# Kernel optimization log

Hardware: AMD Instinct MI355X
Metric: run time of the kernel (lower is better)

The kernel has to match this reference:

```python
import jax, jax.numpy as jnp
import numpy as np

# The torch code implements pixel shifts via bmm with sparse permutation
# matrices: T[i,i+1]=1. bmm(x, T) moves column j-1 -> j (shift right, zero col 0);
# bmm(x, T^T) shifts left; bmm(T, x) moves row j+1 -> j (shift up, zero last row);
# bmm(T^T, x) shifts down. We implement these directly as pad+slice gathers.

def _shift_right(x):  # [B,H,W]
    return jnp.pad(x[:, :, :-1], ((0, 0), (0, 0), (1, 0)))

def _shift_left(x):
    return jnp.pad(x[:, :, 1:], ((0, 0), (0, 0), (0, 1)))

def _shift_up(x):
    return jnp.pad(x[:, 1:, :], ((0, 0), (0, 1), (0, 0)))

def _shift_down(x):
    return jnp.pad(x[:, :-1, :], ((0, 0), (1, 0), (0, 0)))

def _bce_sum(p, t):
    # torch.nn.BCELoss(reduction='sum') clamps log terms at -100
    logp = jnp.clip(jnp.log(p), -100.0, None)
    log1mp = jnp.clip(jnp.log1p(-p), -100.0, None)
    return -jnp.sum(t * logp + (1.0 - t) * log1mp)

def setup_inputs() -> dict:
    key = jax.random.key(0)
    k1, k2, k3 = jax.random.split(key, 3)
    B, C, H, W = 16, 8, 512, 512
    c_map = jax.random.normal(k1, (B, C, H, W), dtype=jnp.float32)
    target = jax.random.bernoulli(k2, 0.5, (B, 1, H, W)).astype(jnp.float32)
    con_target = jax.random.bernoulli(k3, 0.5, (B, C, H, W)).astype(jnp.float32)
    return {"c_map": c_map, "target": target, "con_target": con_target}

def reference(c_map, target, con_target):
    p = jax.nn.sigmoid(c_map)  # [B,8,H,W]

    sum_conn = jnp.sum(con_target, axis=1)  # [B,H,W]
    edge = ((sum_conn < 8.0) & (sum_conn > 0.0)).astype(p.dtype)

    c0, c1, c2, c3 = p[:, 0], p[:, 1], p[:, 2], p[:, 3]
    c4, c5, c6, c7 = p[:, 4], p[:, 5], p[:, 6], p[:, 7]

    right = _shift_right(c4)
    left = _shift_left(c3)
    left_bottom = _shift_left(_shift_down(c5))
    right_above = _shift_right(_shift_up(c2))
    left_above = _shift_left(_shift_up(c0))
    bottom = _shift_down(c6)
    up = _shift_up(c1)
    right_bottom = _shift_right(_shift_down(c7))

    a1 = c3 * right
    a2 = c4 * left
    a3 = c1 * bottom
    a4 = c6 * up
    a5 = c2 * left_bottom
    a6 = c5 * right_above
    a7 = c0 * right_bottom
    a8 = c7 * left_above

    vote_out = jnp.stack([a7, a3, a5, a1, a2, a6, a4, a8], axis=1)  # [B,8,H,W]

    glo_map = jnp.mean(vote_out, axis=1)       # [B,H,W]
    pred_mask_min = jnp.min(vote_out, axis=1)  # [B,H,W]
    decouple_map = glo_map * (1.0 - edge) + (1.0 - pred_mask_min) * edge

    de_loss = _bce_sum(decouple_map[:, None], target)
    conmap_l = _bce_sum(p, con_target)
    bimap_l = _bce_sum(vote_out, con_target)
    return 0.8 * conmap_l + de_loss + 0.2 * bimap_l
```

## Files before the change

### kernel.cpp

```cpp
#include <hip/hip_runtime.h>
#include <math.h>

#define NB 16
#define NC 8
#define HH 512
#define WW 512
#define HW (HH * WW)
#define CHW (NC * HW)

typedef const __attribute__((address_space(1))) void* gvp;
typedef __attribute__((address_space(3))) void*       lvp;

__device__ __forceinline__ float sigf(float x) {
    return __fdividef(1.0f, 1.0f + __expf(-x));
}

__device__ __forceinline__ float bce_term(float t, float p) {
    float q = (t > 0.5f) ? p : (1.0f - p);
    return -fmaxf(__logf(q), -100.0f);
}

__device__ __forceinline__ void ld4(const float* p, float* o) {
    float4 v = *(const float4*)p;
    o[0] = v.x; o[1] = v.y; o[2] = v.z; o[3] = v.w;
}

__global__ __launch_bounds__(256) void bicon_loss_kernel(
    const float* __restrict__ c_map,
    const float* __restrict__ target,
    const float* __restrict__ con_target,
    float* __restrict__ out)
{
    __shared__ float lds[22][WW];

    const int b    = blockIdx.x >> 8;
    const int h0   = (blockIdx.x & 255) << 1;
    const int tid  = threadIdx.x;
    const int wave = tid >> 6;
    const int lane = tid & 63;

    for (int s = wave; s < 44; s += 4) {
        const int plane = s >> 1, half = s & 1;
        int ch, rel;
        if      (plane < 3)  { ch = 5 + plane;  rel = -1; }
        else if (plane < 11) { ch = plane - 3;  rel = 0;  }
        else if (plane < 19) { ch = plane - 11; rel = 1;  }
        else                 { ch = plane - 19; rel = 2;  }
        int rr = h0 + rel;
        rr = rr < 0 ? 0 : (rr > HH - 1 ? HH - 1 : rr);
        const float* gp = c_map + b * CHW + ch * HW + rr * WW + half * 256 + lane * 4;
        __builtin_amdgcn_global_load_lds((gvp)gp, (lvp)&lds[plane][half * 256], 16, 0, 0);
    }

    const int r   = tid >> 7;
    const int px0 = (tid & 127) << 2;
    const int gr  = h0 + r;

    const float* ct = con_target + b * CHW + gr * WW + px0;
    float tv[8][4];
    #pragma unroll
    for (int c = 0; c < 8; ++c) ld4(ct + c * HW, tv[c]);
    float tg[4];
    ld4(target + b * HW + gr * WW + px0, tg);

    __syncthreads();

    const bool hu = gr > 0, hd = gr < HH - 1;
    const bool wl = px0 > 0, wr = px0 < WW - 4;

    const int cb = r ? 11 : 3;
    const int pu5 = r ? 8 : 0, pu6 = r ? 9 : 1, pu7 = r ? 10 : 2;
    const int pd0 = r ? 19 : 11, pd1 = r ? 20 : 12, pd2 = r ? 21 : 13;

    float sp[8][4];
    #pragma unroll
    for (int c = 0; c < 8; ++c) {
        float cv[4]; ld4(&lds[cb + c][px0], cv);
        #pragma unroll
        for (int j = 0; j < 4; ++j) sp[c][j] = sigf(cv[j]);
    }

    float u5[4], u6[4], u7[4], dd0[4], dd1[4], dd2[4];
    ld4(&lds[pu5][px0], u5);
    ld4(&lds[pu6][px0], u6);
    ld4(&lds[pu7][px0], u7);
    ld4(&lds[pd0][px0], dd0);
    ld4(&lds[pd1][px0], dd1);
    ld4(&lds[pd2][px0], dd2);
    const float e5  = lds[pu5][wr ? px0 + 4 : px0];
    const float e7  = lds[pu7][wl ? px0 - 1 : px0];
    const float e2  = lds[pd2][wr ? px0 + 4 : px0];
    const float e0  = lds[pd0][wl ? px0 - 1 : px0];
    const float m4e = lds[cb + 4][wl ? px0 - 1 : px0];
    const float m3e = lds[cb + 3][wr ? px0 + 4 : px0];

    float acc_con = 0.0f, acc_bi = 0.0f, acc_de = 0.0f;
    #pragma unroll
    for (int j = 0; j < 4; ++j) {
        const float n6  = hu ? sigf(u6[j]) : 0.0f;
        const float n5  = (j < 3) ? (hu ? sigf(u5[j + 1]) : 0.0f)
                                  : ((hu && wr) ? sigf(e5) : 0.0f);
        const float n7  = (j > 0) ? (hu ? sigf(u7[j - 1]) : 0.0f)
                                  : ((hu && wl) ? sigf(e7) : 0.0f);
        const float dn1 = hd ? sigf(dd1[j]) : 0.0f;
        const float dn2 = (j < 3) ? (hd ? sigf(dd2[j + 1]) : 0.0f)
                                  : ((hd && wr) ? sigf(e2) : 0.0f);
        const float dn0 = (j > 0) ? (hd ? sigf(dd0[j - 1]) : 0.0f)
                                  : ((hd && wl) ? sigf(e0) : 0.0f);
        const float m4  = (j > 0) ? sp[4][j - 1] : (wl ? sigf(m4e) : 0.0f);
        const float m3  = (j < 3) ? sp[3][j + 1] : (wr ? sigf(m3e) : 0.0f);

        const float a1 = sp[3][j] * m4;
        const float a2 = sp[4][j] * m3;
        const float a3 = sp[1][j] * n6;
        const float a4 = sp[6][j] * dn1;
        const float a5 = sp[2][j] * n5;
        const float a6 = sp[5][j] * dn2;
        const float a7 = sp[0][j] * n7;
        const float a8 = sp[7][j] * dn0;

        const float vote[8] = { a7, a3, a5, a1, a2, a6, a4, a8 };

        float sum_conn = 0.0f;
        #pragma unroll
        for (int c = 0; c < 8; ++c) sum_conn += tv[c][j];

        #pragma unroll
        for (int c = 0; c < 8; ++c) {
            acc_con += bce_term(tv[c][j], sp[c][j]);
            acc_bi  += bce_term(tv[c][j], vote[c]);
        }

        const float glo = (a1 + a2 + a3 + a4 + a5 + a6 + a7 + a8) * 0.125f;
        float mn = vote[0];
        #pragma unroll
        for (int c = 1; c < 8; ++c) mn = fminf(mn, vote[c]);

        const bool edge = (sum_conn < 8.0f) && (sum_conn > 0.0f);
        const float dec = edge ? (1.0f - mn) : glo;
        acc_de += bce_term(tg[j], dec);
    }

    float local = fmaf(0.8f, acc_con, fmaf(0.2f, acc_bi, acc_de));

    #pragma unroll
    for (int off = 32; off > 0; off >>= 1)
        local += __shfl_down(local, off, 64);

    __shared__ float wsum[4];
    if (lane == 0) wsum[wave] = local;
    __syncthreads();
    if (tid == 0) {
        atomicAdd(out, wsum[0] + wsum[1] + wsum[2] + wsum[3]);
    }
}

extern "C" void kernel_launch(void* const* d_in, const int* in_sizes, int n_in,
                              void* d_out, int out_size, void* d_ws, size_t ws_size,
                              hipStream_t stream) {
    const float* c_map      = (const float*)d_in[0];
    const float* target     = (const float*)d_in[1];
    const float* con_target = (const float*)d_in[2];
    float* out = (float*)d_out;

    hipMemsetAsync(out, 0, sizeof(float), stream);

    const int blocks = NB * (HH / 2);
    bicon_loss_kernel<<<blocks, 256, 0, stream>>>(c_map, target, con_target, out);
}
```

Before: 292.2 us.

## Compute sigmoid once per pixel, share via LDS, use log2-domain BCE

Each thread now loads its own-row c_map values straight into registers and computes the sigmoid once, while LDS staging is cut to the six neighbour-row planes (which are sigmoided in place). Own-row sigmoids needed by the other row are written back to LDS, behind an extra barrier. The conmap BCE is rewritten algebraically as log(1+e^-x) plus x for negative targets, and all logs are taken in base 2 with one final ln2 scale. Launch bounds request 4 blocks per CU and LDS use drops. The aim is to remove the redundant sigmoid and log work of neighbour lookups, at the cost of an extra sync and slightly different clamp and rounding behaviour.

```diff
diff --git a/kernel.cpp b/kernel.cpp
--- a/kernel.cpp
+++ b/kernel.cpp
@@ -8,6 +8,10 @@
 #define HW (HH * WW)
 #define CHW (NC * HW)
 
+#define LOG2E 1.44269504088896f
+#define LN2   0.693147180559945f
+#define CLMP  144.269504088896f
+
 typedef const __attribute__((address_space(1))) void* gvp;
 typedef __attribute__((address_space(3))) void*       lvp;
 
@@ -15,9 +19,9 @@
     return __fdividef(1.0f, 1.0f + __expf(-x));
 }
 
-__device__ __forceinline__ float bce_term(float t, float p) {
-    float q = (t > 0.5f) ? p : (1.0f - p);
-    return -fmaxf(__logf(q), -100.0f);
+__device__ __forceinline__ float bce2(float t, float v) {
+    float q = (t > 0.5f) ? v : (1.0f - v);
+    return fminf(-__builtin_amdgcn_logf(q), CLMP);
 }
 
 __device__ __forceinline__ void ld4(const float* p, float* o) {
@@ -25,13 +29,13 @@
     o[0] = v.x; o[1] = v.y; o[2] = v.z; o[3] = v.w;
 }
 
-__global__ __launch_bounds__(256) void bicon_loss_kernel(
+__global__ __launch_bounds__(256, 4) void bicon_loss_kernel(
     const float* __restrict__ c_map,
     const float* __restrict__ target,
     const float* __restrict__ con_target,
     float* __restrict__ out)
 {
-    __shared__ float lds[22][WW];
+    __shared__ float lds[16][WW];
 
     const int b    = blockIdx.x >> 8;
     const int h0   = (blockIdx.x & 255) << 1;
@@ -39,14 +43,11 @@
     const int wave = tid >> 6;
     const int lane = tid & 63;
 
-    for (int s = wave; s < 44; s += 4) {
+    for (int s = wave; s < 12; s += 4) {
         const int plane = s >> 1, half = s & 1;
-        int ch, rel;
-        if      (plane < 3)  { ch = 5 + plane;  rel = -1; }
-        else if (plane < 11) { ch = plane - 3;  rel = 0;  }
-        else if (plane < 19) { ch = plane - 11; rel = 1;  }
-        else                 { ch = plane - 19; rel = 2;  }
-        int rr = h0 + rel;
+        int ch, rr;
+        if (plane < 3) { ch = 5 + plane; rr = h0 - 1; }
+        else           { ch = plane - 3; rr = h0 + 2; }
         rr = rr < 0 ? 0 : (rr > HH - 1 ? HH - 1 : rr);
         const float* gp = c_map + b * CHW + ch * HW + rr * WW + half * 256 + lane * 4;
         __builtin_amdgcn_global_load_lds((gvp)gp, (lvp)&lds[plane][half * 256], 16, 0, 0);
@@ -56,6 +57,11 @@
     const int px0 = (tid & 127) << 2;
     const int gr  = h0 + r;
 
+    const float* cm = c_map + b * CHW + gr * WW + px0;
+    float cv[8][4];
+    #pragma unroll
+    for (int c = 0; c < 8; ++c) ld4(cm + c * HW, cv[c]);
+
     const float* ct = con_target + b * CHW + gr * WW + px0;
     float tv[8][4];
     #pragma unroll
@@ -65,20 +71,50 @@
 
     __syncthreads();
 
+    #pragma unroll
+    for (int k = 0; k < 3; ++k) {
+        float4* lp = reinterpret_cast<float4*>(&lds[0][0]) + (k * 256 + tid);
+        float4 v = *lp;
+        v.x = sigf(v.x); v.y = sigf(v.y); v.z = sigf(v.z); v.w = sigf(v.w);
+        *lp = v;
+    }
+
+    float sp[8][4];
+    float acc_con = 0.0f;
+    #pragma unroll
+    for (int c = 0; c < 8; ++c) {
+        #pragma unroll
+        for (int j = 0; j < 4; ++j) {
+            const float cl2 = cv[c][j] * LOG2E;
+            const float e   = __builtin_amdgcn_exp2f(-cl2);
+            const float s   = 1.0f + e;
+            const float Lg  = __builtin_amdgcn_logf(s);
+            sp[c][j] = __builtin_amdgcn_rcpf(s);
+            const float extra = (tv[c][j] > 0.5f) ? 0.0f : cl2;
+            acc_con += fminf(Lg + extra, CLMP);
+        }
+    }
+
+    if (r == 0) {
+        #pragma unroll
+        for (int c = 3; c < 8; ++c)
+            *(float4*)&lds[3 + c][px0] =
+                make_float4(sp[c][0], sp[c][1], sp[c][2], sp[c][3]);
+    } else {
+        #pragma unroll
+        for (int c = 0; c < 5; ++c)
+            *(float4*)&lds[11 + c][px0] =
+                make_float4(sp[c][0], sp[c][1], sp[c][2], sp[c][3]);
+    }
+
+    __syncthreads();
+
     const bool hu = gr > 0, hd = gr < HH - 1;
     const bool wl = px0 > 0, wr = px0 < WW - 4;
 
-    const int cb = r ? 11 : 3;
-    const int pu5 = r ? 8 : 0, pu6 = r ? 9 : 1, pu7 = r ? 10 : 2;
-    const int pd0 = r ? 19 : 11, pd1 = r ? 20 : 12, pd2 = r ? 21 : 13;
-
-    float sp[8][4];
-    #pragma unroll
-    for (int c = 0; c < 8; ++c) {
-        float cv[4]; ld4(&lds[cb + c][px0], cv);
-        #pragma unroll
-        for (int j = 0; j < 4; ++j) sp[c][j] = sigf(cv[j]);
-    }
+    const int pu5 = r ? 8 : 0,  pu6 = r ? 9 : 1,  pu7 = r ? 10 : 2;
+    const int pd0 = r ? 3 : 11, pd1 = r ? 4 : 12, pd2 = r ? 5 : 13;
+    const int pe3 = r ? 14 : 6, pe4 = r ? 15 : 7;
 
     float u5[4], u6[4], u7[4], dd0[4], dd1[4], dd2[4];
     ld4(&lds[pu5][px0], u5);
@@ -91,24 +127,24 @@
     const float e7  = lds[pu7][wl ? px0 - 1 : px0];
     const float e2  = lds[pd2][wr ? px0 + 4 : px0];
     const float e0  = lds[pd0][wl ? px0 - 1 : px0];
-    const float m4e = lds[cb + 4][wl ? px0 - 1 : px0];
-    const float m3e = lds[cb + 3][wr ? px0 + 4 : px0];
-
-    float acc_con = 0.0f, acc_bi = 0.0f, acc_de = 0.0f;
+    const float m4e = lds[pe4][wl ? px0 - 1 : px0];
+    const float m3e = lds[pe3][wr ? px0 + 4 : px0];
+
+    float acc_bi = 0.0f, acc_de = 0.0f;
     #pragma unroll
     for (int j = 0; j < 4; ++j) {
-        const float n6  = hu ? sigf(u6[j]) : 0.0f;
-        const float n5  = (j < 3) ? (hu ? sigf(u5[j + 1]) : 0.0f)
-                                  : ((hu && wr) ? sigf(e5) : 0.0f);
-        const float n7  = (j > 0) ? (hu ? sigf(u7[j - 1]) : 0.0f)
-                                  : ((hu && wl) ? sigf(e7) : 0.0f);
-        const float dn1 = hd ? sigf(dd1[j]) : 0.0f;
-        const float dn2 = (j < 3) ? (hd ? sigf(dd2[j + 1]) : 0.0f)
-                                  : ((hd && wr) ? sigf(e2) : 0.0f);
-        const float dn0 = (j > 0) ? (hd ? sigf(dd0[j - 1]) : 0.0f)
-                                  : ((hd && wl) ? sigf(e0) : 0.0f);
-        const float m4  = (j > 0) ? sp[4][j - 1] : (wl ? sigf(m4e) : 0.0f);
-        const float m3  = (j < 3) ? sp[3][j + 1] : (wr ? sigf(m3e) : 0.0f);
+        const float n6  = hu ? u6[j] : 0.0f;
+        const float n5  = (j < 3) ? (hu ? u5[j + 1] : 0.0f)
+                                  : ((hu && wr) ? e5 : 0.0f);
+        const float n7  = (j > 0) ? (hu ? u7[j - 1] : 0.0f)
+                                  : ((hu && wl) ? e7 : 0.0f);
+        const float dn1 = hd ? dd1[j] : 0.0f;
+        const float dn2 = (j < 3) ? (hd ? dd2[j + 1] : 0.0f)
+                                  : ((hd && wr) ? e2 : 0.0f);
+        const float dn0 = (j > 0) ? (hd ? dd0[j - 1] : 0.0f)
+                                  : ((hd && wl) ? e0 : 0.0f);
+        const float m4  = (j > 0) ? sp[4][j - 1] : (wl ? m4e : 0.0f);
+        const float m3  = (j < 3) ? sp[3][j + 1] : (wr ? m3e : 0.0f);
 
         const float a1 = sp[3][j] * m4;
         const float a2 = sp[4][j] * m3;
@@ -126,10 +162,7 @@
         for (int c = 0; c < 8; ++c) sum_conn += tv[c][j];
 
         #pragma unroll
-        for (int c = 0; c < 8; ++c) {
-            acc_con += bce_term(tv[c][j], sp[c][j]);
-            acc_bi  += bce_term(tv[c][j], vote[c]);
-        }
+        for (int c = 0; c < 8; ++c) acc_bi += bce2(tv[c][j], vote[c]);
 
         const float glo = (a1 + a2 + a3 + a4 + a5 + a6 + a7 + a8) * 0.125f;
         float mn = vote[0];
@@ -138,21 +171,20 @@
 
         const bool edge = (sum_conn < 8.0f) && (sum_conn > 0.0f);
         const float dec = edge ? (1.0f - mn) : glo;
-        acc_de += bce_term(tg[j], dec);
-    }
-
-    float local = fmaf(0.8f, acc_con, fmaf(0.2f, acc_bi, acc_de));
+        acc_de += bce2(tg[j], dec);
+    }
+
+    float local = fmaf(0.8f, acc_con, fmaf(0.2f, acc_bi, acc_de)) * LN2;
 
     #pragma unroll
     for (int off = 32; off > 0; off >>= 1)
         local += __shfl_down(local, off, 64);
 
-    __shared__ float wsum[4];
-    if (lane == 0) wsum[wave] = local;
-    __syncthreads();
-    if (tid == 0) {
-        atomicAdd(out, wsum[0] + wsum[1] + wsum[2] + wsum[3]);
-    }
+    __syncthreads();
+    if (lane == 0) lds[0][wave] = local;
+    __syncthreads();
+    if (tid == 0)
+        atomicAdd(out, (lds[0][0] + lds[0][1]) + (lds[0][2] + lds[0][3]));
 }
 
 extern "C" void kernel_launch(void* const* d_in, const int* in_sizes, int n_in,
```

Result: slower. 300.7 us (+2.9%).

## Replace LDS staging with direct loads, wave shuffles and log2-domain BCE

Applied to the files above, without the earlier changes.

Drops the LDS staging buffer and the block barrier. Each thread now loads its own row and neighbour rows straight from global memory and gets horizontal neighbours through wave shuffles, with single-element loads at wave edges. The BCE math is rewritten in the log2 domain: the conmap loss comes from log(1+exp(-x)) without a divide, and the targets are packed into a bitmask that drives both the edge test and term selection. The aim is to cut LDS traffic, sync and transcendental cost, in exchange for more redundant global loads of neighbour rows served by cache.

```diff
diff --git a/kernel.cpp b/kernel.cpp
--- a/kernel.cpp
+++ b/kernel.cpp
@@ -8,16 +8,12 @@
 #define HW (HH * WW)
 #define CHW (NC * HW)
 
-typedef const __attribute__((address_space(1))) void* gvp;
-typedef __attribute__((address_space(3))) void*       lvp;
+#define LOG2E 1.44269504088896f
+#define LN2   0.693147180559945f
+#define CLMP  144.269504088896f
 
 __device__ __forceinline__ float sigf(float x) {
-    return __fdividef(1.0f, 1.0f + __expf(-x));
-}
-
-__device__ __forceinline__ float bce_term(float t, float p) {
-    float q = (t > 0.5f) ? p : (1.0f - p);
-    return -fmaxf(__logf(q), -100.0f);
+    return __builtin_amdgcn_rcpf(1.0f + __builtin_amdgcn_exp2f(-x * LOG2E));
 }
 
 __device__ __forceinline__ void ld4(const float* p, float* o) {
@@ -25,90 +21,99 @@
     o[0] = v.x; o[1] = v.y; o[2] = v.z; o[3] = v.w;
 }
 
-__global__ __launch_bounds__(256) void bicon_loss_kernel(
+__global__ __launch_bounds__(256, 4) void bicon_loss_kernel(
     const float* __restrict__ c_map,
     const float* __restrict__ target,
     const float* __restrict__ con_target,
     float* __restrict__ out)
 {
-    __shared__ float lds[22][WW];
+    const int tid  = threadIdx.x;
+    const int lane = tid & 63;
+    const int wave = tid >> 6;
+    const int t    = blockIdx.x * 256 + tid;
+    const int g    = t >> 7;
+    const int b    = g >> 9;
+    const int row  = g & 511;
+    const int px0  = (t & 127) << 2;
 
-    const int b    = blockIdx.x >> 8;
-    const int h0   = (blockIdx.x & 255) << 1;
-    const int tid  = threadIdx.x;
-    const int wave = tid >> 6;
-    const int lane = tid & 63;
+    const bool hu = row > 0, hd = row < HH - 1;
+    const bool wl = px0 > 0, wr = px0 < WW - 4;
+    const int rU = hu ? row - 1 : 0;
+    const int rD = hd ? row + 1 : HH - 1;
 
-    for (int s = wave; s < 44; s += 4) {
-        const int plane = s >> 1, half = s & 1;
-        int ch, rel;
-        if      (plane < 3)  { ch = 5 + plane;  rel = -1; }
-        else if (plane < 11) { ch = plane - 3;  rel = 0;  }
-        else if (plane < 19) { ch = plane - 11; rel = 1;  }
-        else                 { ch = plane - 19; rel = 2;  }
-        int rr = h0 + rel;
-        rr = rr < 0 ? 0 : (rr > HH - 1 ? HH - 1 : rr);
-        const float* gp = c_map + b * CHW + ch * HW + rr * WW + half * 256 + lane * 4;
-        __builtin_amdgcn_global_load_lds((gvp)gp, (lvp)&lds[plane][half * 256], 16, 0, 0);
+    const float* base = c_map + b * CHW;
+    const int ro = row * WW + px0;
+
+    float u5r[4], u6r[4], u7r[4], d0r[4], d1r[4], d2r[4];
+    ld4(base + 5 * HW + rU * WW + px0, u5r);
+    ld4(base + 6 * HW + rU * WW + px0, u6r);
+    ld4(base + 7 * HW + rU * WW + px0, u7r);
+    ld4(base + 0 * HW + rD * WW + px0, d0r);
+    ld4(base + 1 * HW + rD * WW + px0, d1r);
+    ld4(base + 2 * HW + rD * WW + px0, d2r);
+
+    float tg[4];
+    ld4(target + b * HW + ro, tg);
+
+    const bool atL = (lane == 0)  && wl;
+    const bool atR = (lane == 63) && wr;
+    float eL7 = 0.f, eL0 = 0.f, eL4 = 0.f, eR5 = 0.f, eR2 = 0.f, eR3 = 0.f;
+    if (atL) {
+        eL7 = base[7 * HW + rU  * WW + px0 - 1];
+        eL0 = base[0 * HW + rD  * WW + px0 - 1];
+        eL4 = base[4 * HW + row * WW + px0 - 1];
+    }
+    if (atR) {
+        eR5 = base[5 * HW + rU  * WW + px0 + 4];
+        eR2 = base[2 * HW + rD  * WW + px0 + 4];
+        eR3 = base[3 * HW + row * WW + px0 + 4];
     }
 
-    const int r   = tid >> 7;
-    const int px0 = (tid & 127) << 2;
-    const int gr  = h0 + r;
-
-    const float* ct = con_target + b * CHW + gr * WW + px0;
-    float tv[8][4];
-    #pragma unroll
-    for (int c = 0; c < 8; ++c) ld4(ct + c * HW, tv[c]);
-    float tg[4];
-    ld4(target + b * HW + gr * WW + px0, tg);
-
-    __syncthreads();
-
-    const bool hu = gr > 0, hd = gr < HH - 1;
-    const bool wl = px0 > 0, wr = px0 < WW - 4;
-
-    const int cb = r ? 11 : 3;
-    const int pu5 = r ? 8 : 0, pu6 = r ? 9 : 1, pu7 = r ? 10 : 2;
-    const int pd0 = r ? 19 : 11, pd1 = r ? 20 : 12, pd2 = r ? 21 : 13;
-
+    const float* cm = base + ro;
+    const float* ct = con_target + b * CHW + ro;
     float sp[8][4];
+    int msk[4] = {0, 0, 0, 0};
+    float acc_con = 0.0f;
     #pragma unroll
     for (int c = 0; c < 8; ++c) {
-        float cv[4]; ld4(&lds[cb + c][px0], cv);
+        float cv4[4], tvc[4];
+        ld4(cm + c * HW, cv4);
+        ld4(ct + c * HW, tvc);
         #pragma unroll
-        for (int j = 0; j < 4; ++j) sp[c][j] = sigf(cv[j]);
+        for (int j = 0; j < 4; ++j) {
+            const float cl2 = cv4[j] * LOG2E;
+            const float e   = __builtin_amdgcn_exp2f(-cl2);
+            const float s   = 1.0f + e;
+            const float Lg  = __builtin_amdgcn_logf(s);
+            sp[c][j] = __builtin_amdgcn_rcpf(s);
+            const bool one = tvc[j] > 0.5f;
+            msk[j] |= (int)one << c;
+            acc_con += fminf(Lg + (one ? 0.0f : cl2), CLMP);
+        }
     }
 
-    float u5[4], u6[4], u7[4], dd0[4], dd1[4], dd2[4];
-    ld4(&lds[pu5][px0], u5);
-    ld4(&lds[pu6][px0], u6);
-    ld4(&lds[pu7][px0], u7);
-    ld4(&lds[pd0][px0], dd0);
-    ld4(&lds[pd1][px0], dd1);
-    ld4(&lds[pd2][px0], dd2);
-    const float e5  = lds[pu5][wr ? px0 + 4 : px0];
-    const float e7  = lds[pu7][wl ? px0 - 1 : px0];
-    const float e2  = lds[pd2][wr ? px0 + 4 : px0];
-    const float e0  = lds[pd0][wl ? px0 - 1 : px0];
-    const float m4e = lds[cb + 4][wl ? px0 - 1 : px0];
-    const float m3e = lds[cb + 3][wr ? px0 + 4 : px0];
+    float u5n = __shfl_down(u5r[0], 1, 64); if (lane == 63) u5n = eR5;
+    float u7p = __shfl_up (u7r[3], 1, 64); if (lane == 0)  u7p = eL7;
+    float d2n = __shfl_down(d2r[0], 1, 64); if (lane == 63) d2n = eR2;
+    float d0p = __shfl_up (d0r[3], 1, 64); if (lane == 0)  d0p = eL0;
+    float sp4p = __shfl_up (sp[4][3], 1, 64); if (lane == 0)  sp4p = sigf(eL4);
+    float sp3n = __shfl_down(sp[3][0], 1, 64); if (lane == 63) sp3n = sigf(eR3);
 
-    float acc_con = 0.0f, acc_bi = 0.0f, acc_de = 0.0f;
+    float acc_bi = 0.0f, acc_de = 0.0f;
     #pragma unroll
     for (int j = 0; j < 4; ++j) {
-        const float n6  = hu ? sigf(u6[j]) : 0.0f;
-        const float n5  = (j < 3) ? (hu ? sigf(u5[j + 1]) : 0.0f)
-                                  : ((hu && wr) ? sigf(e5) : 0.0f);
-        const float n7  = (j > 0) ? (hu ? sigf(u7[j - 1]) : 0.0f)
-                                  : ((hu && wl) ? sigf(e7) : 0.0f);
-        const float dn1 = hd ? sigf(dd1[j]) : 0.0f;
-        const float dn2 = (j < 3) ? (hd ? sigf(dd2[j + 1]) : 0.0f)
-                                  : ((hd && wr) ? sigf(e2) : 0.0f);
-        const float dn0 = (j > 0) ? (hd ? sigf(dd0[j - 1]) : 0.0f)
-                                  : ((hd && wl) ? sigf(e0) : 0.0f);
-        const float m4  = (j > 0) ? sp[4][j - 1] : (wl ? sigf(m4e) : 0.0f);
-        const float m3  = (j < 3) ? sp[3][j + 1] : (wr ? sigf(m3e) : 0.0f);
+        const float n6  = hu ? sigf(u6r[j]) : 0.0f;
+        const float n5  = (((j < 3) ? hu : (hu && wr)))
+                          ? sigf((j < 3) ? u5r[j + 1] : u5n) : 0.0f;
+        const float n7  = (((j > 0) ? hu : (hu && wl)))
+                          ? sigf((j > 0) ? u7r[j - 1] : u7p) : 0.0f;
+        const float dn1 = hd ? sigf(d1r[j]) : 0.0f;
+        const float dn2 = (((j < 3) ? hd : (hd && wr)))
+                          ? sigf((j < 3) ? d2r[j + 1] : d2n) : 0.0f;
+        const float dn0 = (((j > 0) ? hd : (hd && wl)))
+                          ? sigf((j > 0) ? d0r[j - 1] : d0p) : 0.0f;
+        const float m4  = (j > 0) ? sp[4][j - 1] : (wl ? sp4p : 0.0f);
+        const float m3  = (j < 3) ? sp[3][j + 1] : (wr ? sp3n : 0.0f);
 
         const float a1 = sp[3][j] * m4;
         const float a2 = sp[4][j] * m3;
@@ -120,15 +125,13 @@
         const float a8 = sp[7][j] * dn0;
 
         const float vote[8] = { a7, a3, a5, a1, a2, a6, a4, a8 };
-
-        float sum_conn = 0.0f;
-        #pragma unroll
-        for (int c = 0; c < 8; ++c) sum_conn += tv[c][j];
+        const int m = msk[j];
 
         #pragma unroll
         for (int c = 0; c < 8; ++c) {
-            acc_con += bce_term(tv[c][j], sp[c][j]);
-            acc_bi  += bce_term(tv[c][j], vote[c]);
+            const bool one = (m >> c) & 1;
+            const float q = one ? vote[c] : (1.0f - vote[c]);
+            acc_bi += fminf(-__builtin_amdgcn_logf(q), CLMP);
         }
 
         const float glo = (a1 + a2 + a3 + a4 + a5 + a6 + a7 + a8) * 0.125f;
@@ -136,12 +139,13 @@
         #pragma unroll
         for (int c = 1; c < 8; ++c) mn = fminf(mn, vote[c]);
 
-        const bool edge = (sum_conn < 8.0f) && (sum_conn > 0.0f);
+        const bool edge = (m != 0) && (m != 255);
         const float dec = edge ? (1.0f - mn) : glo;
-        acc_de += bce_term(tg[j], dec);
+        const float qd  = (tg[j] > 0.5f) ? dec : (1.0f - dec);
+        acc_de += fminf(-__builtin_amdgcn_logf(qd), CLMP);
     }
 
-    float local = fmaf(0.8f, acc_con, fmaf(0.2f, acc_bi, acc_de));
+    float local = fmaf(0.8f, acc_con, fmaf(0.2f, acc_bi, acc_de)) * LN2;
 
     #pragma unroll
     for (int off = 32; off > 0; off >>= 1)
@@ -150,9 +154,8 @@
     __shared__ float wsum[4];
     if (lane == 0) wsum[wave] = local;
     __syncthreads();
-    if (tid == 0) {
-        atomicAdd(out, wsum[0] + wsum[1] + wsum[2] + wsum[3]);
-    }
+    if (tid == 0)
+        atomicAdd(out, (wsum[0] + wsum[1]) + (wsum[2] + wsum[3]));
 }
 
 extern "C" void kernel_launch(void* const* d_in, const int* in_sizes, int n_in,
```

New measurement: 288.4 us. About the same (-1.3%).
